# Optimization experiments

Hardware: AMD Instinct MI355X
Metric: run time of the kernel (lower is better)

The kernel has to match this reference:

```python
import jax, jax.numpy as jnp
import numpy as np

HIDDEN_DIM = 1024
SEQ_LEN = 4096
D_IN = 1024


def setup_inputs() -> dict:
    key = jax.random.key(0)
    ks = jax.random.split(key, 9)
    s = 1.0 / np.sqrt(D_IN)
    return {
        "q": jax.random.normal(ks[0], (SEQ_LEN, D_IN), jnp.float32),
        "k": jax.random.normal(ks[1], (SEQ_LEN, D_IN), jnp.float32),
        "v": jax.random.normal(ks[2], (SEQ_LEN, D_IN), jnp.float32),
        "Wq": jax.random.normal(ks[3], (D_IN, HIDDEN_DIM), jnp.float32) * s,
        "bq": jnp.zeros((HIDDEN_DIM,), jnp.float32),
        "Wk": jax.random.normal(ks[4], (D_IN, HIDDEN_DIM), jnp.float32) * s,
        "bk": jnp.zeros((HIDDEN_DIM,), jnp.float32),
        "Wv": jax.random.normal(ks[5], (D_IN, HIDDEN_DIM), jnp.float32) * s,
        "bv": jnpp_zeros() if False else jnp.zeros((HIDDEN_DIM,), jnp.float32),
    }


def reference(q, k, v, Wq, bq, Wk, bk, Wv, bv):
    # Dense projections (flax Dense: x @ W + b)
    query = q @ Wq + bq          # [S, H]
    key_p = k @ Wk + bk          # [S, H]
    value = v @ Wv + bv          # [S, H]
    # scores = Q K^T / sqrt(hidden_dim)  -> [S, S]
    scores = jnp.matmul(query, key_p.T) / jnp.sqrt(jnp.float32(HIDDEN_DIM))
    weights = jax.nn.softmax(scores, axis=-1)
    context = jnp.matmul(weights, value)  # [S, H]
    return context
```

## Files before the change

### kernel.cpp

```cpp
#include <hip/hip_runtime.h>


typedef short short4v __attribute__((ext_vector_type(4)));
typedef short short8  __attribute__((ext_vector_type(8)));
typedef float f32x4   __attribute__((ext_vector_type(4)));

#define MFMA16 __builtin_amdgcn_mfma_f32_16x16x32_bf16

__device__ __forceinline__ short f2bf(float f) {
    union { float f; unsigned u; } x; x.f = f;
    unsigned r = (x.u + 0x7FFFu + ((x.u >> 16) & 1u)) >> 16;
    return (short)r;
}
__device__ __forceinline__ float bf2f(short s) {
    union { unsigned u; float f; } x;
    x.u = ((unsigned)(unsigned short)s) << 16; return x.f;
}

__device__ __forceinline__ void gl2lds(const short* g, short* l) {
    __builtin_amdgcn_global_load_lds(
        (const __attribute__((address_space(1))) void*)g,
        (__attribute__((address_space(3))) void*)l, 16, 0, 0);
}

__global__ __launch_bounds__(256) void prep_w(
    const float* __restrict__ W0, const float* __restrict__ W1,
    const float* __restrict__ W2, short* __restrict__ Wt)
{
    __shared__ float tile[64][65];
    const float* W = blockIdx.z == 0 ? W0 : (blockIdx.z == 1 ? W1 : W2);
    short* T = Wt + (size_t)blockIdx.z * 1048576;
    const int c0 = blockIdx.x * 64;
    const int r0 = blockIdx.y * 64;
    const int tx = threadIdx.x & 63;
    const int ty = threadIdx.x >> 6;
    #pragma unroll
    for (int p = 0; p < 16; ++p) {
        int r = ty + p * 4;
        tile[r][tx] = W[(size_t)(r0 + r) * 1024 + c0 + tx];
    }
    __syncthreads();
    #pragma unroll
    for (int p = 0; p < 16; ++p) {
        int r = ty + p * 4;
        T[(size_t)(c0 + r) * 1024 + r0 + tx] = f2bf(tile[tx][r]);
    }
}

__global__ __launch_bounds__(256) void cast_qkv(
    const float* __restrict__ q, const float* __restrict__ k,
    const float* __restrict__ v, short* __restrict__ xb)
{
    const float* src = blockIdx.z == 0 ? q : (blockIdx.z == 1 ? k : v);
    short* dst = xb + (size_t)blockIdx.z * 4194304;
    for (int i = blockIdx.x * 256 + threadIdx.x; i < 1048576; i += 256 * 1024) {
        float4 f = ((const float4*)src)[i];
        short4v o;
        o[0] = f2bf(f.x); o[1] = f2bf(f.y); o[2] = f2bf(f.z); o[3] = f2bf(f.w);
        ((short4v*)dst)[i] = o;
    }
}

template <typename TOut, int MODE>
__global__ __launch_bounds__(512, 4) void gemm128(
    const short* __restrict__ A, const short* __restrict__ Bt,
    const float* __restrict__ b0, const float* __restrict__ b1,
    const float* __restrict__ b2,
    TOut* __restrict__ C, float* __restrict__ P1, float* __restrict__ P2,
    float* __restrict__ P3, short* __restrict__ Vt,
    int M, int N, int lda, int ldb, float scale,
    int nc, int nc_last, int kstep)
{
    __shared__ short Lds[24576];

    const int t    = threadIdx.x;
    const int lane = t & 63;
    const int wv   = t >> 6;

    const int nb  = gridDim.x;
    const int bid = blockIdx.y * nb + blockIdx.x;
    const int band   = bid / (8 * nb);
    const int within = bid - band * 8 * nb;
    const int m0 = (band * 8 + (within & 7)) * 128;
    const int n0 = (within >> 3) * 256;

    const float* bias = nullptr;
    int kbeg = 0;
    TOut* Cw = C;
    if constexpr (MODE == 1) {
        const int z = blockIdx.z;
        A  += (size_t)z * M * lda;
        Bt += (size_t)z * N * ldb;
        Cw  = C + (size_t)(z < 2 ? z : 0) * M * N;
        bias = z == 0 ? b0 : (z == 1 ? b1 : b2);
    }
    if constexpr (MODE == 2) {
        const int z = blockIdx.z;
        kbeg = z * kstep;
        if (z == (int)gridDim.z - 1) nc = nc_last;
        Cw = (TOut*)(z == 0 ? (float*)C : (z == 1 ? P1 : (z == 2 ? P2 : P3)));
    }
    (void)b0; (void)b1; (void)b2; (void)P1; (void)P2; (void)P3; (void)Vt;
    (void)nc_last; (void)kstep;

    const int srow = lane >> 2;
    const int skof = ((lane & 3) ^ ((lane >> 3) & 3)) * 8;
    const short* pA  = A  + (size_t)(m0 + wv * 16 + srow) * lda + kbeg + skof;
    const short* pB0 = Bt + (size_t)(n0 + wv * 16 + srow) * ldb + kbeg + skof;
    const short* pB1 = pB0 + (size_t)128 * ldb;
    short* sA  = Lds + wv * 512;
    short* sB0 = Lds + 4096 + wv * 512;
    short* sB1 = Lds + 8192 + wv * 512;

    const int wm = wv >> 2, wn = wv & 3;
    const int lr = lane & 15, lq = lane >> 4;
    const int pcol = lq ^ ((lr >> 1) & 3);
    const short* rdA = Lds + (wm * 64 + lr) * 32 + pcol * 8;
    const short* rdB = Lds + 4096 + (wn * 64 + lr) * 32 + pcol * 8;

    f32x4 acc[4][4];
    #pragma unroll
    for (int i = 0; i < 4; ++i)
        #pragma unroll
        for (int j = 0; j < 4; ++j) { f32x4 z4 = {0.f,0.f,0.f,0.f}; acc[i][j] = z4; }

#define STAGE(c) {                                                        \
    const int s_ = (c) & 1;                                               \
    const size_t ko_ = (size_t)(c) * 32;                                  \
    gl2lds(pA  + ko_, sA  + s_ * 12288);                                  \
    gl2lds(pB0 + ko_, sB0 + s_ * 12288);                                  \
    gl2lds(pB1 + ko_, sB1 + s_ * 12288); }

#define COMPUTE(c) {                                                      \
    const short* rA_ = rdA + ((c) & 1) * 12288;                           \
    const short* rB_ = rdB + ((c) & 1) * 12288;                           \
    short8 af[4], bf_[4];                                                 \
    _Pragma("unroll") for (int i = 0; i < 4; ++i)                         \
        af[i] = *(const short8*)(rA_ + i * 512);                          \
    _Pragma("unroll") for (int j = 0; j < 4; ++j)                         \
        bf_[j] = *(const short8*)(rB_ + j * 512);                         \
    __builtin_amdgcn_s_setprio(1);                                        \
    _Pragma("unroll") for (int i = 0; i < 4; ++i)                         \
        _Pragma("unroll") for (int j = 0; j < 4; ++j)                     \
            acc[i][j] = MFMA16(af[i], bf_[j], acc[i][j], 0, 0, 0);        \
    __builtin_amdgcn_s_setprio(0); }

    STAGE(0);

    for (int c = 0; c < nc - 1; ++c) {
        STAGE(c + 1);
        asm volatile("s_waitcnt vmcnt(3)" ::: "memory");
        __builtin_amdgcn_s_barrier();
        COMPUTE(c);
        __builtin_amdgcn_s_barrier();
    }
    asm volatile("s_waitcnt vmcnt(0)" ::: "memory");
    __builtin_amdgcn_s_barrier();
    COMPUTE(nc - 1);
#undef COMPUTE
#undef STAGE

    if constexpr (MODE == 1) {
        if (blockIdx.z == 2) {
            #pragma unroll
            for (int hh = 0; hh < 4; ++hh) {
                __syncthreads();
                if (wn == hh) {
                    #pragma unroll
                    for (int i = 0; i < 4; ++i) {
                        #pragma unroll
                        for (int j = 0; j < 4; ++j) {
                            const int colL = j * 16 + lr;
                            const float bb = bias[n0 + hh * 64 + colL];
                            #pragma unroll
                            for (int r = 0; r < 4; ++r) {
                                const int rowL = wm * 64 + i * 16 + lq * 4 + r;
                                Lds[colL * 136 + rowL] =
                                    f2bf(acc[i][j][r] * scale + bb);
                            }
                        }
                    }
                }
                __syncthreads();
                const int c = t >> 3, part = t & 7;
                short* dst = Vt + (size_t)(n0 + hh * 64 + c) * 4096
                                + m0 + part * 16;
                const short* src = &Lds[c * 136 + part * 16];
                *(short8*)dst       = *(const short8*)src;
                *(short8*)(dst + 8) = *(const short8*)(src + 8);
            }
            return;
        }
    }

    if constexpr (sizeof(TOut) == 2) {
        #pragma unroll
        for (int p = 0; p < 2; ++p) {
            __syncthreads();
            if (wm == p) {
                #pragma unroll
                for (int i = 0; i < 4; ++i) {
                    #pragma unroll
                    for (int j = 0; j < 4; ++j) {
                        const int col = wn * 64 + j * 16 + lr;
                        float bb = 0.f;
                        if constexpr (MODE == 1) bb = bias[n0 + col];
                        #pragma unroll
                        for (int r = 0; r < 4; ++r) {
                            const int row = i * 16 + lq * 4 + r;
                            Lds[row * 272 + col] =
                                f2bf(acc[i][j][r] * scale + bb);
                        }
                    }
                }
            }
            __syncthreads();
            const int row = t >> 3, part = t & 7;
            short* dst = (short*)Cw + (size_t)(m0 + p * 64 + row) * N
                          + n0 + part * 32;
            const short* src = &Lds[row * 272 + part * 32];
            #pragma unroll
            for (int s = 0; s < 4; ++s)
                ((short8*)dst)[s] = ((const short8*)src)[s];
        }
        return;
    }

    #pragma unroll
    for (int i = 0; i < 4; ++i) {
        const int crow = m0 + wm * 64 + i * 16 + lq * 4;
        #pragma unroll
        for (int j = 0; j < 4; ++j) {
            const int ccol = n0 + wn * 64 + j * 16 + lr;
            #pragma unroll
            for (int r = 0; r < 4; ++r)
                Cw[(size_t)(crow + r) * N + ccol] = acc[i][j][r] * scale;
        }
    }
}

__global__ __launch_bounds__(256) void softmax_bf16(short* __restrict__ S)
{
    const int row = blockIdx.x;
    short8* r8 = (short8*)(S + (size_t)row * 4096);
    const int t = threadIdx.x;

    float x[16];
    #pragma unroll
    for (int i = 0; i < 2; ++i) {
        short8 raw = r8[t + 256 * i];
        #pragma unroll
        for (int j = 0; j < 8; ++j) x[8 * i + j] = bf2f(raw[j]);
    }
    float m = -1e30f;
    #pragma unroll
    for (int i = 0; i < 16; ++i) m = fmaxf(m, x[i]);
    #pragma unroll
    for (int off = 32; off > 0; off >>= 1) m = fmaxf(m, __shfl_xor(m, off));

    __shared__ float redm[4], reds[4];
    const int wv = t >> 6;
    if ((t & 63) == 0) redm[wv] = m;
    __syncthreads();
    m = fmaxf(fmaxf(redm[0], redm[1]), fmaxf(redm[2], redm[3]));

    float s = 0.f;
    #pragma unroll
    for (int i = 0; i < 16; ++i) { x[i] = __expf(x[i] - m); s += x[i]; }
    #pragma unroll
    for (int off = 32; off > 0; off >>= 1) s += __shfl_xor(s, off);
    if ((t & 63) == 0) reds[wv] = s;
    __syncthreads();
    s = reds[0] + reds[1] + reds[2] + reds[3];
    const float inv = 1.f / s;

    #pragma unroll
    for (int i = 0; i < 2; ++i) {
        short8 o;
        #pragma unroll
        for (int j = 0; j < 8; ++j) o[j] = f2bf(x[8 * i + j] * inv);
        r8[t + 256 * i] = o;
    }
}

__global__ __launch_bounds__(256) void combine(
    float* __restrict__ out, const float* __restrict__ a,
    const float* __restrict__ b, const float* __restrict__ c, int np)
{
    for (int i = blockIdx.x * 256 + threadIdx.x; i < 1048576; i += 256 * 1024) {
        float4 o = ((const float4*)out)[i];
        float4 x = ((const float4*)a)[i];
        float4 y = ((const float4*)b)[i];
        o.x += x.x + y.x; o.y += x.y + y.y;
        o.z += x.z + y.z; o.w += x.w + y.w;
        if (np == 3) {
            float4 w = ((const float4*)c)[i];
            o.x += w.x; o.y += w.y; o.z += w.z; o.w += w.w;
        }
        ((float4*)out)[i] = o;
    }
}

extern "C" void kernel_launch(void* const* d_in, const int* in_sizes, int n_in,
                              void* d_out, int out_size, void* d_ws, size_t ws_size,
                              hipStream_t stream)
{
    const float* q  = (const float*)d_in[0];
    const float* k  = (const float*)d_in[1];
    const float* v  = (const float*)d_in[2];
    const float* Wq = (const float*)d_in[3];
    const float* bq = (const float*)d_in[4];
    const float* Wk = (const float*)d_in[5];
    const float* bk = (const float*)d_in[6];
    const float* Wv = (const float*)d_in[7];
    const float* bv = (const float*)d_in[8];
    float* out = (float*)d_out;

    char* ws = (char*)d_ws;
    const size_t MB = 1ull << 20;
    short* Wt = (short*)(ws + 0);
    short* xb = (short*)(ws + 6 * MB);
    short* pr = (short*)(ws + 30 * MB);
    short* S  = (short*)(ws + 46 * MB);
    short* Vt = (short*)(ws + 78 * MB);
    float* p1 = (float*)(ws + 0);
    float* p2 = (float*)(ws + 16 * MB);
    float* p3 = (float*)(ws + 86 * MB);
    const int SK = (ws_size >= 102 * MB) ? 4 : 3;

    prep_w<<<dim3(16, 16, 3), 256, 0, stream>>>(Wq, Wk, Wv, Wt);
    cast_qkv<<<dim3(1024, 1, 3), 256, 0, stream>>>(q, k, v, xb);
    gemm128<short, 1><<<dim3(4, 32, 3), 512, 0, stream>>>(
        xb, Wt, bq, bk, bv, pr, nullptr, nullptr, nullptr, Vt,
        4096, 1024, 1024, 1024, 1.f, 32, 32, 0);
    gemm128<short, 0><<<dim3(16, 32), 512, 0, stream>>>(
        pr, pr + 4 * 1024 * 1024, nullptr, nullptr, nullptr, S,
        nullptr, nullptr, nullptr, nullptr,
        4096, 4096, 1024, 1024, 0.03125f, 32, 32, 0);
    softmax_bf16<<<4096, 256, 0, stream>>>(S);
    if (SK == 4) {
        gemm128<float, 2><<<dim3(4, 32, 4), 512, 0, stream>>>(
            S, Vt, nullptr, nullptr, nullptr, out, p1, p2, p3, nullptr,
            4096, 1024, 4096, 4096, 1.f, 32, 32, 1024);
        combine<<<1024, 256, 0, stream>>>(out, p1, p2, p3, 3);
    } else {
        gemm128<float, 2><<<dim3(4, 32, 3), 512, 0, stream>>>(
            S, Vt, nullptr, nullptr, nullptr, out, p1, p2, nullptr, nullptr,
            4096, 1024, 4096, 4096, 1.f, 42, 44, 1344);
        combine<<<1024, 256, 0, stream>>>(out, p1, p2, nullptr, 2);
    }
}
```

Measured before the change: 262.8 us.

## Fuse fp32-to-bf16 input cast into projection GEMM and simplify bf16 epilogue

Removes the separate cast_qkv kernel. The projection GEMM now reads fp32 q/k/v directly, converts each A chunk to bf16 in registers and writes it to LDS, with extra lgkmcnt waits before the barrier. This saves a full write and re-read of the bf16 activation copies, but the A operand is now a register round-trip instead of an asynchronous global-to-LDS load. The LDS-staged, coalesced bf16 output epilogue is also replaced with direct per-lane 2-byte stores, which may write the large score matrix less efficiently.

```diff
diff --git a/kernel.cpp b/kernel.cpp
--- a/kernel.cpp
+++ b/kernel.cpp
@@ -47,23 +47,10 @@
     }
 }
 
-__global__ __launch_bounds__(256) void cast_qkv(
-    const float* __restrict__ q, const float* __restrict__ k,
-    const float* __restrict__ v, short* __restrict__ xb)
-{
-    const float* src = blockIdx.z == 0 ? q : (blockIdx.z == 1 ? k : v);
-    short* dst = xb + (size_t)blockIdx.z * 4194304;
-    for (int i = blockIdx.x * 256 + threadIdx.x; i < 1048576; i += 256 * 1024) {
-        float4 f = ((const float4*)src)[i];
-        short4v o;
-        o[0] = f2bf(f.x); o[1] = f2bf(f.y); o[2] = f2bf(f.z); o[3] = f2bf(f.w);
-        ((short4v*)dst)[i] = o;
-    }
-}
-
-template <typename TOut, int MODE>
+template <typename TIn, typename TOut, int MODE>
 __global__ __launch_bounds__(512, 4) void gemm128(
-    const short* __restrict__ A, const short* __restrict__ Bt,
+    const TIn* __restrict__ A0, const TIn* __restrict__ A1,
+    const TIn* __restrict__ A2, const short* __restrict__ Bt,
     const float* __restrict__ b0, const float* __restrict__ b1,
     const float* __restrict__ b2,
     TOut* __restrict__ C, float* __restrict__ P1, float* __restrict__ P2,
@@ -84,12 +71,13 @@
     const int m0 = (band * 8 + (within & 7)) * 128;
     const int n0 = (within >> 3) * 256;
 
+    const TIn* A = A0;
     const float* bias = nullptr;
     int kbeg = 0;
     TOut* Cw = C;
     if constexpr (MODE == 1) {
         const int z = blockIdx.z;
-        A  += (size_t)z * M * lda;
+        A = z == 0 ? A0 : (z == 1 ? A1 : A2);
         Bt += (size_t)z * N * ldb;
         Cw  = C + (size_t)(z < 2 ? z : 0) * M * N;
         bias = z == 0 ? b0 : (z == 1 ? b1 : b2);
@@ -100,17 +88,18 @@
         if (z == (int)gridDim.z - 1) nc = nc_last;
         Cw = (TOut*)(z == 0 ? (float*)C : (z == 1 ? P1 : (z == 2 ? P2 : P3)));
     }
-    (void)b0; (void)b1; (void)b2; (void)P1; (void)P2; (void)P3; (void)Vt;
-    (void)nc_last; (void)kstep;
+    (void)A1; (void)A2; (void)b0; (void)b1; (void)b2;
+    (void)P1; (void)P2; (void)P3; (void)Vt; (void)nc_last; (void)kstep;
 
     const int srow = lane >> 2;
     const int skof = ((lane & 3) ^ ((lane >> 3) & 3)) * 8;
-    const short* pA  = A  + (size_t)(m0 + wv * 16 + srow) * lda + kbeg + skof;
+    const TIn*  pA  = A  + (size_t)(m0 + wv * 16 + srow) * lda + kbeg + skof;
     const short* pB0 = Bt + (size_t)(n0 + wv * 16 + srow) * ldb + kbeg + skof;
     const short* pB1 = pB0 + (size_t)128 * ldb;
     short* sA  = Lds + wv * 512;
     short* sB0 = Lds + 4096 + wv * 512;
     short* sB1 = Lds + 8192 + wv * 512;
+    short* sAw = Lds + wv * 512 + lane * 8;
 
     const int wm = wv >> 2, wn = wv & 3;
     const int lr = lane & 15, lq = lane >> 4;
@@ -124,12 +113,27 @@
         #pragma unroll
         for (int j = 0; j < 4; ++j) { f32x4 z4 = {0.f,0.f,0.f,0.f}; acc[i][j] = z4; }
 
-#define STAGE(c) {                                                        \
+#define STAGE_CHUNK(c) {                                                  \
     const int s_ = (c) & 1;                                               \
     const size_t ko_ = (size_t)(c) * 32;                                  \
-    gl2lds(pA  + ko_, sA  + s_ * 12288);                                  \
-    gl2lds(pB0 + ko_, sB0 + s_ * 12288);                                  \
-    gl2lds(pB1 + ko_, sB1 + s_ * 12288); }
+    if constexpr (sizeof(TIn) == 4) {                                     \
+                  \
+        const float* asrc_ = (const float*)pA + ko_;                      \
+        float4 fa0_ = *(const float4*)asrc_;                              \
+        float4 fa1_ = *(const float4*)(asrc_ + 4);                        \
+        gl2lds(pB0 + ko_, sB0 + s_ * 12288);                              \
+        gl2lds(pB1 + ko_, sB1 + s_ * 12288);                              \
+        short8 o_;                                                        \
+        o_[0] = f2bf(fa0_.x); o_[1] = f2bf(fa0_.y);                       \
+        o_[2] = f2bf(fa0_.z); o_[3] = f2bf(fa0_.w);                       \
+        o_[4] = f2bf(fa1_.x); o_[5] = f2bf(fa1_.y);                       \
+        o_[6] = f2bf(fa1_.z); o_[7] = f2bf(fa1_.w);                       \
+        *(short8*)(sAw + s_ * 12288) = o_;                                \
+    } else {                                                              \
+        gl2lds((const short*)pA + ko_, sA + s_ * 12288);                  \
+        gl2lds(pB0 + ko_, sB0 + s_ * 12288);                              \
+        gl2lds(pB1 + ko_, sB1 + s_ * 12288);                              \
+    } }
 
 #define COMPUTE(c) {                                                      \
     const short* rA_ = rdA + ((c) & 1) * 12288;                           \
@@ -145,20 +149,27 @@
             acc[i][j] = MFMA16(af[i], bf_[j], acc[i][j], 0, 0, 0);        \
     __builtin_amdgcn_s_setprio(0); }
 
-    STAGE(0);
+    STAGE_CHUNK(0);
 
     for (int c = 0; c < nc - 1; ++c) {
-        STAGE(c + 1);
-        asm volatile("s_waitcnt vmcnt(3)" ::: "memory");
+        STAGE_CHUNK(c + 1);
+        if constexpr (sizeof(TIn) == 4) {
+            asm volatile("s_waitcnt vmcnt(2)" ::: "memory");
+            asm volatile("s_waitcnt lgkmcnt(0)" ::: "memory");
+        } else {
+            asm volatile("s_waitcnt vmcnt(3)" ::: "memory");
+        }
         __builtin_amdgcn_s_barrier();
         COMPUTE(c);
         __builtin_amdgcn_s_barrier();
     }
     asm volatile("s_waitcnt vmcnt(0)" ::: "memory");
+    if constexpr (sizeof(TIn) == 4)
+        asm volatile("s_waitcnt lgkmcnt(0)" ::: "memory");
     __builtin_amdgcn_s_barrier();
     COMPUTE(nc - 1);
 #undef COMPUTE
-#undef STAGE
+#undef STAGE_CHUNK
 
     if constexpr (MODE == 1) {
         if (blockIdx.z == 2) {
@@ -193,48 +204,22 @@
         }
     }
 
-    if constexpr (sizeof(TOut) == 2) {
-        #pragma unroll
-        for (int p = 0; p < 2; ++p) {
-            __syncthreads();
-            if (wm == p) {
-                #pragma unroll
-                for (int i = 0; i < 4; ++i) {
-                    #pragma unroll
-                    for (int j = 0; j < 4; ++j) {
-                        const int col = wn * 64 + j * 16 + lr;
-                        float bb = 0.f;
-                        if constexpr (MODE == 1) bb = bias[n0 + col];
-                        #pragma unroll
-                        for (int r = 0; r < 4; ++r) {
-                            const int row = i * 16 + lq * 4 + r;
-                            Lds[row * 272 + col] =
-                                f2bf(acc[i][j][r] * scale + bb);
-                        }
-                    }
-                }
-            }
-            __syncthreads();
-            const int row = t >> 3, part = t & 7;
-            short* dst = (short*)Cw + (size_t)(m0 + p * 64 + row) * N
-                          + n0 + part * 32;
-            const short* src = &Lds[row * 272 + part * 32];
-            #pragma unroll
-            for (int s = 0; s < 4; ++s)
-                ((short8*)dst)[s] = ((const short8*)src)[s];
-        }
-        return;
-    }
-
     #pragma unroll
     for (int i = 0; i < 4; ++i) {
         const int crow = m0 + wm * 64 + i * 16 + lq * 4;
         #pragma unroll
         for (int j = 0; j < 4; ++j) {
             const int ccol = n0 + wn * 64 + j * 16 + lr;
+            float bb = 0.f;
+            if constexpr (MODE == 1) bb = bias[ccol];
             #pragma unroll
-            for (int r = 0; r < 4; ++r)
-                Cw[(size_t)(crow + r) * N + ccol] = acc[i][j][r] * scale;
+            for (int r = 0; r < 4; ++r) {
+                float val = acc[i][j][r] * scale + bb;
+                if constexpr (sizeof(TOut) == 2)
+                    ((short*)Cw)[(size_t)(crow + r) * N + ccol] = f2bf(val);
+                else
+                    ((float*)Cw)[(size_t)(crow + r) * N + ccol] = val;
+            }
         }
     }
 }
@@ -319,7 +304,6 @@
     char* ws = (char*)d_ws;
     const size_t MB = 1ull << 20;
     short* Wt = (short*)(ws + 0);
-    short* xb = (short*)(ws + 6 * MB);
     short* pr = (short*)(ws + 30 * MB);
     short* S  = (short*)(ws + 46 * MB);
     short* Vt = (short*)(ws + 78 * MB);
@@ -329,23 +313,24 @@
     const int SK = (ws_size >= 102 * MB) ? 4 : 3;
 
     prep_w<<<dim3(16, 16, 3), 256, 0, stream>>>(Wq, Wk, Wv, Wt);
-    cast_qkv<<<dim3(1024, 1, 3), 256, 0, stream>>>(q, k, v, xb);
-    gemm128<short, 1><<<dim3(4, 32, 3), 512, 0, stream>>>(
-        xb, Wt, bq, bk, bv, pr, nullptr, nullptr, nullptr, Vt,
+    gemm128<float, short, 1><<<dim3(4, 32, 3), 512, 0, stream>>>(
+        q, k, v, Wt, bq, bk, bv, pr, nullptr, nullptr, nullptr, Vt,
         4096, 1024, 1024, 1024, 1.f, 32, 32, 0);
-    gemm128<short, 0><<<dim3(16, 32), 512, 0, stream>>>(
-        pr, pr + 4 * 1024 * 1024, nullptr, nullptr, nullptr, S,
-        nullptr, nullptr, nullptr, nullptr,
+    gemm128<short, short, 0><<<dim3(16, 32), 512, 0, stream>>>(
+        pr, nullptr, nullptr, pr + 4 * 1024 * 1024,
+        nullptr, nullptr, nullptr, S, nullptr, nullptr, nullptr, nullptr,
         4096, 4096, 1024, 1024, 0.03125f, 32, 32, 0);
     softmax_bf16<<<4096, 256, 0, stream>>>(S);
     if (SK == 4) {
-        gemm128<float, 2><<<dim3(4, 32, 4), 512, 0, stream>>>(
-            S, Vt, nullptr, nullptr, nullptr, out, p1, p2, p3, nullptr,
+        gemm128<short, float, 2><<<dim3(4, 32, 4), 512, 0, stream>>>(
+            S, nullptr, nullptr, Vt, nullptr, nullptr, nullptr,
+            out, p1, p2, p3, nullptr,
             4096, 1024, 4096, 4096, 1.f, 32, 32, 1024);
         combine<<<1024, 256, 0, stream>>>(out, p1, p2, p3, 3);
     } else {
-        gemm128<float, 2><<<dim3(4, 32, 3), 512, 0, stream>>>(
-            S, Vt, nullptr, nullptr, nullptr, out, p1, p2, nullptr, nullptr,
+        gemm128<short, float, 2><<<dim3(4, 32, 3), 512, 0, stream>>>(
+            S, nullptr, nullptr, Vt, nullptr, nullptr, nullptr,
+            out, p1, p2, nullptr, nullptr,
             4096, 1024, 4096, 4096, 1.f, 42, 44, 1344);
         combine<<<1024, 256, 0, stream>>>(out, p1, p2, nullptr, 2);
     }
```

Measured after the change: 261.1 us. Within noise of the previous version (-0.6%).
